# Optimization experiments

Measured on AMD Instinct MI355X. Metric: run time of the kernel, lower is better.

## Reference

```python
import jax, jax.numpy as jnp
import numpy as np

B, T, E = 4, 2048, 1024
N, P = 16, 64  # num_heads, projection_dim = E // N
SCALE = P ** 0.5


def setup_inputs() -> dict:
    key = jax.random.key(0)
    k1, k2, k3 = jax.random.split(key, 3)
    x = jax.random.normal(k1, (B, T, E), dtype=jnp.float32)
    w_qkv = jax.random.normal(k2, (E, N, 3 * P), dtype=jnp.float32) * 0.02
    b_qkv = jnp.zeros((N, 3 * P), dtype=jnp.float32)
    w_o = jax.random.normal(k3, (P, N, E), dtype=jnp.float32) * 0.02
    b_o = jnp.zeros((E,), dtype=jnp.float32)
    return {"x": x, "w_qkv": w_qkv, "b_qkv": b_qkv, "w_o": w_o, "b_o": b_o}


def reference(x, w_qkv, b_qkv, w_o, b_o):
    # QKV projection: bte,enp->btnp (+ bias over n,p)
    qkv = jnp.einsum('bte,enp->btnp', x, w_qkv) + b_qkv  # [B,T,N,3P]
    qkv = jnp.transpose(qkv, (0, 2, 1, 3))               # [B,N,T,3P]
    q, k, v = jnp.split(qkv, 3, axis=-1)                 # each [B,N,T,P]
    scores = jnp.einsum('bnip,bnjp->bnij', q, k) / SCALE # [B,N,T,T]
    attn = jax.nn.softmax(scores, axis=-1)
    weighted = jnp.einsum('bnij,bnjp->bnip', attn, v)    # [B,N,T,P]
    # Output projection: bntp,pne->bte (+ bias over e)
    out = jnp.einsum('bntp,pne->bte', weighted, w_o) + b_o
    return out
```

## Files before the change

kernel.cpp:

```cpp
#include <hip/hip_runtime.h>

typedef __attribute__((ext_vector_type(8))) short bf16x8;
typedef __attribute__((ext_vector_type(4))) short s16x4;
typedef __attribute__((ext_vector_type(4))) float f32x4;
typedef __attribute__((ext_vector_type(2))) unsigned u32x2;

#define MFMA16(a,b,c) __builtin_amdgcn_mfma_f32_16x16x32_bf16((a),(b),(c),0,0,0)

static constexpr int Bsz = 4, T = 2048, E = 1024, NH = 16, HP = 64;
static constexpr int J3 = NH * 3 * HP;

__device__ __forceinline__ short f2bf(float f) {
  union { float f; unsigned u; } v; v.f = f;
  unsigned r = (v.u + 0x7fffu + ((v.u >> 16) & 1u)) >> 16;
  return (short)r;
}

__device__ __forceinline__ unsigned cvtpk(float a, float b) {
  unsigned r;
  asm("v_cvt_pk_bf16_f32 %0, %1, %2" : "=v"(r) : "v"(a), "v"(b));
  return r;
}

typedef __attribute__((address_space(3))) unsigned int lds_u32;
typedef __attribute__((address_space(1))) const unsigned int glb_u32;
__device__ __forceinline__ void gl16(const short* g, const short* l) {
  __builtin_amdgcn_global_load_lds((glb_u32*)g, (lds_u32*)l, 16, 0, 0);
}

__global__ void cvt_x(const float4* __restrict__ x, s16x4* __restrict__ xb) {
  int i = blockIdx.x * 256 + threadIdx.x;
  float4 v = x[i];
  s16x4 r;
  r[0] = f2bf(v.x); r[1] = f2bf(v.y); r[2] = f2bf(v.z); r[3] = f2bf(v.w);
  xb[i] = r;
}

__global__ void cvt_wqkv(const float* __restrict__ w, short* __restrict__ wt) {
  __shared__ float tile[32][33];
  int jb = blockIdx.x * 32, eb = blockIdx.y * 32;
  int tx = threadIdx.x & 31, ty = threadIdx.x >> 5;
  for (int r = 0; r < 32; r += 8)
    tile[ty + r][tx] = w[(size_t)(eb + ty + r) * J3 + jb + tx];
  __syncthreads();
  for (int r = 0; r < 32; r += 8)
    wt[(size_t)(jb + ty + r) * E + eb + tx] = f2bf(tile[tx][ty + r]);
}

__global__ void cvt_wo(const float* __restrict__ w, short* __restrict__ wt) {
  int o = blockIdx.x * 256 + threadIdx.x;
  int e = o >> 10, k = o & 1023;
  int n = k >> 6, p = k & 63;
  wt[o] = f2bf(w[(size_t)(p * 16 + n) * E + e]);
}

__global__ __launch_bounds__(256) void gemm_qkv(
    const short* __restrict__ A,
    const short* __restrict__ Bt,
    const float* __restrict__ bias,
    short* __restrict__ Qb, short* __restrict__ Kb, short* __restrict__ Vt) {
  __shared__ short As[128 * 64];
  __shared__ short Bs[128 * 64];
  const int m0 = blockIdx.x * 128, n0 = blockIdx.y * 128;
  const int tid = threadIdx.x;
  const int lane = tid & 63, w = tid >> 6;
  const int wm = (w >> 1) * 64, wn = (w & 1) * 64;
  const int l15 = lane & 15, lh = lane >> 4;
  const int l7 = l15 & 7;

  const int rA = lane >> 3;
  const int cS = 8 * ((lane & 7) ^ rA);
  const short* Ap = A + (size_t)(m0 + w * 32 + rA) * 1024 + cS;
  const short* Bp = Bt + (size_t)(n0 + w * 32 + rA) * 1024 + cS;
  const short* AsBase = As + w * 2048;
  const short* BsBase = Bs + w * 2048;

  f32x4 acc[4][4] = {};

  for (int k0 = 0; k0 < 1024; k0 += 64) {
    __syncthreads();
#pragma unroll
    for (int j = 0; j < 4; j++) {
      gl16(Ap + j * 8192 + k0, AsBase + j * 512);
      gl16(Bp + j * 8192 + k0, BsBase + j * 512);
    }
    __syncthreads();
    bf16x8 af[2][4], bfr[2][4];
#pragma unroll
    for (int kk = 0; kk < 2; kk++) {
#pragma unroll
      for (int m = 0; m < 4; m++)
        af[kk][m] = *(const bf16x8*)(As + (wm + m * 16 + l15) * 64 + 8 * ((kk * 4 + lh) ^ l7));
#pragma unroll
      for (int n = 0; n < 4; n++)
        bfr[kk][n] = *(const bf16x8*)(Bs + (wn + n * 16 + l15) * 64 + 8 * ((kk * 4 + lh) ^ l7));
    }
#pragma unroll
    for (int m = 0; m < 4; m++)
#pragma unroll
      for (int n = 0; n < 4; n++) {
        acc[m][n] = MFMA16(af[0][m], bfr[0][n], acc[m][n]);
        acc[m][n] = MFMA16(af[1][m], bfr[1][n], acc[m][n]);
      }
  }

#pragma unroll
  for (int nn = 0; nn < 4; nn++) {
    int j = n0 + wn + nn * 16 + l15;
    int nh = j / 192, c = j - nh * 192;
    int ty = c >> 6, p = c & 63;
    float bv = bias[j];
#pragma unroll
    for (int mm = 0; mm < 4; mm++) {
#pragma unroll
      for (int r = 0; r < 4; r++) {
        int i = m0 + wm + mm * 16 + lh * 4 + r;
        int bb = i >> 11, tt = i & 2047;
        float val = acc[mm][nn][r] + bv;
        size_t qk = (((size_t)(bb * 16 + nh) * 2048 + tt) << 6) + p;
        if (ty == 0)      Qb[qk] = f2bf(val * 0.180336880f);
        else if (ty == 1) Kb[qk] = f2bf(val);
        else Vt[(((size_t)(bb * 16 + nh) << 6) + p) * 2048 + tt] = f2bf(val);
      }
    }
  }
}

__global__ __launch_bounds__(512, 4) void attn(
    const short* __restrict__ Qb, const short* __restrict__ Kb,
    const short* __restrict__ Vt, short* __restrict__ Wt) {
  __shared__ short Kl[2][64 * 64];
  __shared__ short Vl[2][64 * 64];
  __shared__ short Pl[8][2][16 * 64];
  const int bid = blockIdx.x;
  const int bn = bid & 63, qc = bid >> 6;
  const int tid = threadIdx.x, lane = tid & 63, w = tid >> 6;
  const int l15 = lane & 15, lh = lane >> 4;
  const int l7 = l15 & 7;
  const int q0 = qc * 256 + w * 32;

  const short* Qp = Qb + ((size_t)bn * 2048 + q0) * 64;
  const int rA = lane >> 3;
  const int cS = 8 * ((lane & 7) ^ rA);
  const short* Kg = Kb + (size_t)bn * 2048 * 64 + (w * 8 + rA) * 64 + cS;
  const short* Vg = Vt + (size_t)bn * 64 * 2048 + (size_t)(w * 8 + rA) * 2048 + cS;

  bf16x8 qf[2][2];
#pragma unroll
  for (int qg = 0; qg < 2; qg++)
#pragma unroll
    for (int c = 0; c < 2; c++)
      qf[qg][c] = *(const bf16x8*)(Qp + (qg * 16 + l15) * 64 + c * 32 + 8 * lh);

  float m[2] = {-1e30f, -1e30f}, l[2] = {0.f, 0.f};
  f32x4 o[4][2] = {};
  const f32x4 zero = {0.f, 0.f, 0.f, 0.f};

  gl16(Kg, &Kl[0][w * 512]);
  gl16(Vg, &Vl[0][w * 512]);
  __syncthreads();

  for (int t = 0; t < 32; t++) {
    const int cur = t & 1;
    if (t < 31) {
      gl16(Kg + (t + 1) * 4096, &Kl[cur ^ 1][w * 512]);
      gl16(Vg + (t + 1) * 64,   &Vl[cur ^ 1][w * 512]);
    }
    const short* Kc = &Kl[cur][0];
    const short* Vc = &Vl[cur][0];

    f32x4 s[4][2];
#pragma unroll
    for (int sub = 0; sub < 4; sub++) {
      const short* kr = Kc + (sub * 16 + l15) * 64;
      bf16x8 k0 = *(const bf16x8*)(kr + 8 * (lh ^ l7));
      bf16x8 k1 = *(const bf16x8*)(kr + 8 * ((4 + lh) ^ l7));
#pragma unroll
      for (int qg = 0; qg < 2; qg++) {
        f32x4 tt = MFMA16(k0, qf[qg][0], zero);
        s[sub][qg] = MFMA16(k1, qf[qg][1], tt);
      }
    }

#pragma unroll
    for (int qg = 0; qg < 2; qg++) {
      float pmax = fmaxf(fmaxf(s[0][qg][0], s[0][qg][1]), fmaxf(s[0][qg][2], s[0][qg][3]));
#pragma unroll
      for (int sub = 1; sub < 4; sub++)
        pmax = fmaxf(pmax, fmaxf(fmaxf(s[sub][qg][0], s[sub][qg][1]),
                                 fmaxf(s[sub][qg][2], s[sub][qg][3])));
      pmax = fmaxf(pmax, __shfl_xor(pmax, 16, 64));
      pmax = fmaxf(pmax, __shfl_xor(pmax, 32, 64));
      if (!__all(pmax - m[qg] <= 8.f)) {
        float mn = fmaxf(m[qg], pmax);
        float corr = __builtin_amdgcn_exp2f(m[qg] - mn);
        m[qg] = mn;
        l[qg] *= corr;
#pragma unroll
        for (int psub = 0; psub < 4; psub++)
#pragma unroll
          for (int r = 0; r < 4; r++) o[psub][qg][r] *= corr;
      }
      char* Pw = (char*)&Pl[w][qg][0] + l15 * 128;
      float ps = 0.f;
#pragma unroll
      for (int sub = 0; sub < 4; sub++) {
        float pv0 = __builtin_amdgcn_exp2f(s[sub][qg][0] - m[qg]);
        float pv1 = __builtin_amdgcn_exp2f(s[sub][qg][1] - m[qg]);
        float pv2 = __builtin_amdgcn_exp2f(s[sub][qg][2] - m[qg]);
        float pv3 = __builtin_amdgcn_exp2f(s[sub][qg][3] - m[qg]);
        ps += (pv0 + pv1) + (pv2 + pv3);
        u32x2 pk = {cvtpk(pv0, pv1), cvtpk(pv2, pv3)};
        *(u32x2*)(Pw + ((sub * 32 + lh * 8) ^ (l7 << 4))) = pk;
      }
      ps += __shfl_xor(ps, 16, 64);
      ps += __shfl_xor(ps, 32, 64);
      l[qg] += ps;
    }

    bf16x8 pa[2][2];
#pragma unroll
    for (int qg = 0; qg < 2; qg++) {
      const short* pr = &Pl[w][qg][0] + l15 * 64;
      pa[qg][0] = *(const bf16x8*)(pr + 8 * (lh ^ l7));
      pa[qg][1] = *(const bf16x8*)(pr + 8 * ((4 + lh) ^ l7));
    }
#pragma unroll
    for (int psub = 0; psub < 4; psub++) {
      const short* vr = Vc + (psub * 16 + l15) * 64;
      bf16x8 v0 = *(const bf16x8*)(vr + 8 * (lh ^ l7));
      bf16x8 v1 = *(const bf16x8*)(vr + 8 * ((4 + lh) ^ l7));
#pragma unroll
      for (int qg = 0; qg < 2; qg++) {
        o[psub][qg] = MFMA16(v0, pa[qg][0], o[psub][qg]);
        o[psub][qg] = MFMA16(v1, pa[qg][1], o[psub][qg]);
      }
    }
    __syncthreads();
  }

  const int bb = bn >> 4, n = bn & 15;
#pragma unroll
  for (int qg = 0; qg < 2; qg++) {
    const float invl = 1.0f / l[qg];
    short* wrow = Wt + (size_t)(bb * 2048 + q0 + qg * 16 + l15) * 1024 + n * 64;
#pragma unroll
    for (int psub = 0; psub < 4; psub++) {
      s16x4 pk;
#pragma unroll
      for (int r = 0; r < 4; r++) pk[r] = f2bf(o[psub][qg][r] * invl);
      *(s16x4*)(wrow + psub * 16 + lh * 4) = pk;
    }
  }
}

__global__ __launch_bounds__(256) void gemm_o(
    const short* __restrict__ A,
    const short* __restrict__ Bt,
    const float* __restrict__ bo,
    float* __restrict__ out) {
  __shared__ short As[128 * 64];
  __shared__ short Bs[128 * 64];
  const int m0 = blockIdx.x * 128, n0 = blockIdx.y * 128;
  const int tid = threadIdx.x;
  const int lane = tid & 63, w = tid >> 6;
  const int wm = (w >> 1) * 64, wn = (w & 1) * 64;
  const int l15 = lane & 15, lh = lane >> 4;
  const int l7 = l15 & 7;

  const int rA = lane >> 3;
  const int cS = 8 * ((lane & 7) ^ rA);
  const short* Ap = A + (size_t)(m0 + w * 32 + rA) * 1024 + cS;
  const short* Bp = Bt + (size_t)(n0 + w * 32 + rA) * 1024 + cS;
  const short* AsBase = As + w * 2048;
  const short* BsBase = Bs + w * 2048;

  f32x4 acc[4][4] = {};

  for (int k0 = 0; k0 < 1024; k0 += 64) {
    __syncthreads();
#pragma unroll
    for (int j = 0; j < 4; j++) {
      gl16(Ap + j * 8192 + k0, AsBase + j * 512);
      gl16(Bp + j * 8192 + k0, BsBase + j * 512);
    }
    __syncthreads();
    bf16x8 af[2][4], bfr[2][4];
#pragma unroll
    for (int kk = 0; kk < 2; kk++) {
#pragma unroll
      for (int m = 0; m < 4; m++)
        af[kk][m] = *(const bf16x8*)(As + (wm + m * 16 + l15) * 64 + 8 * ((kk * 4 + lh) ^ l7));
#pragma unroll
      for (int n = 0; n < 4; n++)
        bfr[kk][n] = *(const bf16x8*)(Bs + (wn + n * 16 + l15) * 64 + 8 * ((kk * 4 + lh) ^ l7));
    }
#pragma unroll
    for (int m = 0; m < 4; m++)
#pragma unroll
      for (int n = 0; n < 4; n++) {
        acc[m][n] = MFMA16(af[0][m], bfr[0][n], acc[m][n]);
        acc[m][n] = MFMA16(af[1][m], bfr[1][n], acc[m][n]);
      }
  }

#pragma unroll
  for (int nn = 0; nn < 4; nn++) {
    int e = n0 + wn + nn * 16 + l15;
    float bv = bo[e];
#pragma unroll
    for (int mm = 0; mm < 4; mm++) {
#pragma unroll
      for (int r = 0; r < 4; r++) {
        int i = m0 + wm + mm * 16 + lh * 4 + r;
        out[(size_t)i * 1024 + e] = acc[mm][nn][r] + bv;
      }
    }
  }
}

extern "C" void kernel_launch(void* const* d_in, const int* in_sizes, int n_in,
                              void* d_out, int out_size, void* d_ws, size_t ws_size,
                              hipStream_t stream) {
  (void)in_sizes; (void)n_in; (void)out_size; (void)ws_size;
  const float* x     = (const float*)d_in[0];
  const float* w_qkv = (const float*)d_in[1];
  const float* b_qkv = (const float*)d_in[2];
  const float* w_o   = (const float*)d_in[3];
  const float* b_o   = (const float*)d_in[4];
  float* out = (float*)d_out;
  char* ws = (char*)d_ws;

  short* xb     = (short*)(ws);
  short* wqkvbT = (short*)(ws + 16777216);
  short* wobT   = (short*)(ws + 23068672);
  short* Qb     = (short*)(ws + 25165824);
  short* Kb     = (short*)(ws + 41943040);
  short* Vt     = (short*)(ws + 58720256);
  short* Wt     = (short*)(ws + 75497472);

  hipLaunchKernelGGL(cvt_x,    dim3(8192),    dim3(256), 0, stream, (const float4*)x, (s16x4*)xb);
  hipLaunchKernelGGL(cvt_wqkv, dim3(96, 32),  dim3(256), 0, stream, w_qkv, wqkvbT);
  hipLaunchKernelGGL(cvt_wo,   dim3(4096),    dim3(256), 0, stream, w_o, wobT);
  hipLaunchKernelGGL(gemm_qkv, dim3(64, 24),  dim3(256), 0, stream, xb, wqkvbT, b_qkv, Qb, Kb, Vt);
  hipLaunchKernelGGL(attn,     dim3(512),     dim3(512), 0, stream, Qb, Kb, Vt, Wt);
  hipLaunchKernelGGL(gemm_o,   dim3(64, 8),   dim3(256), 0, stream, Wt, wobT, b_o, out);
}
```

Baseline: 205.4 us.

## Double-buffer LDS tiles in projection GEMMs and raise MFMA wave priority

```diff
diff --git a/kernel.cpp b/kernel.cpp
--- a/kernel.cpp
+++ b/kernel.cpp
@@ -59,8 +59,8 @@
     const short* __restrict__ Bt,
     const float* __restrict__ bias,
     short* __restrict__ Qb, short* __restrict__ Kb, short* __restrict__ Vt) {
-  __shared__ short As[128 * 64];
-  __shared__ short Bs[128 * 64];
+  __shared__ short As[2][128 * 64];
+  __shared__ short Bs[2][128 * 64];
   const int m0 = blockIdx.x * 128, n0 = blockIdx.y * 128;
   const int tid = threadIdx.x;
   const int lane = tid & 63, w = tid >> 6;
@@ -72,29 +72,39 @@
   const int cS = 8 * ((lane & 7) ^ rA);
   const short* Ap = A + (size_t)(m0 + w * 32 + rA) * 1024 + cS;
   const short* Bp = Bt + (size_t)(n0 + w * 32 + rA) * 1024 + cS;
-  const short* AsBase = As + w * 2048;
-  const short* BsBase = Bs + w * 2048;
 
   f32x4 acc[4][4] = {};
 
-  for (int k0 = 0; k0 < 1024; k0 += 64) {
-    __syncthreads();
-#pragma unroll
-    for (int j = 0; j < 4; j++) {
-      gl16(Ap + j * 8192 + k0, AsBase + j * 512);
-      gl16(Bp + j * 8192 + k0, BsBase + j * 512);
-    }
-    __syncthreads();
+#pragma unroll
+  for (int j = 0; j < 4; j++) {
+    gl16(Ap + j * 8192, &As[0][w * 2048 + j * 512]);
+    gl16(Bp + j * 8192, &Bs[0][w * 2048 + j * 512]);
+  }
+  __syncthreads();
+
+  for (int t = 0; t < 16; t++) {
+    const int cur = t & 1;
+    if (t < 15) {
+      const int k0 = (t + 1) * 64;
+#pragma unroll
+      for (int j = 0; j < 4; j++) {
+        gl16(Ap + j * 8192 + k0, &As[cur ^ 1][w * 2048 + j * 512]);
+        gl16(Bp + j * 8192 + k0, &Bs[cur ^ 1][w * 2048 + j * 512]);
+      }
+    }
+    const short* Ac = &As[cur][0];
+    const short* Bc = &Bs[cur][0];
     bf16x8 af[2][4], bfr[2][4];
 #pragma unroll
     for (int kk = 0; kk < 2; kk++) {
 #pragma unroll
       for (int m = 0; m < 4; m++)
-        af[kk][m] = *(const bf16x8*)(As + (wm + m * 16 + l15) * 64 + 8 * ((kk * 4 + lh) ^ l7));
+        af[kk][m] = *(const bf16x8*)(Ac + (wm + m * 16 + l15) * 64 + 8 * ((kk * 4 + lh) ^ l7));
 #pragma unroll
       for (int n = 0; n < 4; n++)
-        bfr[kk][n] = *(const bf16x8*)(Bs + (wn + n * 16 + l15) * 64 + 8 * ((kk * 4 + lh) ^ l7));
-    }
+        bfr[kk][n] = *(const bf16x8*)(Bc + (wn + n * 16 + l15) * 64 + 8 * ((kk * 4 + lh) ^ l7));
+    }
+    __builtin_amdgcn_s_setprio(1);
 #pragma unroll
     for (int m = 0; m < 4; m++)
 #pragma unroll
@@ -102,6 +112,8 @@
         acc[m][n] = MFMA16(af[0][m], bfr[0][n], acc[m][n]);
         acc[m][n] = MFMA16(af[1][m], bfr[1][n], acc[m][n]);
       }
+    __builtin_amdgcn_s_setprio(0);
+    __syncthreads();
   }
 
 #pragma unroll
@@ -170,6 +182,7 @@
     const short* Vc = &Vl[cur][0];
 
     f32x4 s[4][2];
+    __builtin_amdgcn_s_setprio(1);
 #pragma unroll
     for (int sub = 0; sub < 4; sub++) {
       const short* kr = Kc + (sub * 16 + l15) * 64;
@@ -181,6 +194,7 @@
         s[sub][qg] = MFMA16(k1, qf[qg][1], tt);
       }
     }
+    __builtin_amdgcn_s_setprio(0);
 
 #pragma unroll
     for (int qg = 0; qg < 2; qg++) {
@@ -225,6 +239,7 @@
       pa[qg][0] = *(const bf16x8*)(pr + 8 * (lh ^ l7));
       pa[qg][1] = *(const bf16x8*)(pr + 8 * ((4 + lh) ^ l7));
     }
+    __builtin_amdgcn_s_setprio(1);
 #pragma unroll
     for (int psub = 0; psub < 4; psub++) {
       const short* vr = Vc + (psub * 16 + l15) * 64;
@@ -236,6 +251,7 @@
         o[psub][qg] = MFMA16(v1, pa[qg][1], o[psub][qg]);
       }
     }
+    __builtin_amdgcn_s_setprio(0);
     __syncthreads();
   }
 
@@ -259,8 +275,8 @@
     const short* __restrict__ Bt,
     const float* __restrict__ bo,
     float* __restrict__ out) {
-  __shared__ short As[128 * 64];
-  __shared__ short Bs[128 * 64];
+  __shared__ short As[2][128 * 64];
+  __shared__ short Bs[2][128 * 64];
   const int m0 = blockIdx.x * 128, n0 = blockIdx.y * 128;
   const int tid = threadIdx.x;
   const int lane = tid & 63, w = tid >> 6;
@@ -272,29 +288,39 @@
   const int cS = 8 * ((lane & 7) ^ rA);
   const short* Ap = A + (size_t)(m0 + w * 32 + rA) * 1024 + cS;
   const short* Bp = Bt + (size_t)(n0 + w * 32 + rA) * 1024 + cS;
-  const short* AsBase = As + w * 2048;
-  const short* BsBase = Bs + w * 2048;
 
   f32x4 acc[4][4] = {};
 
-  for (int k0 = 0; k0 < 1024; k0 += 64) {
-    __syncthreads();
-#pragma unroll
-    for (int j = 0; j < 4; j++) {
-      gl16(Ap + j * 8192 + k0, AsBase + j * 512);
-      gl16(Bp + j * 8192 + k0, BsBase + j * 512);
-    }
-    __syncthreads();
+#pragma unroll
+  for (int j = 0; j < 4; j++) {
+    gl16(Ap + j * 8192, &As[0][w * 2048 + j * 512]);
+    gl16(Bp + j * 8192, &Bs[0][w * 2048 + j * 512]);
+  }
+  __syncthreads();
+
+  for (int t = 0; t < 16; t++) {
+    const int cur = t & 1;
+    if (t < 15) {
+      const int k0 = (t + 1) * 64;
+#pragma unroll
+      for (int j = 0; j < 4; j++) {
+        gl16(Ap + j * 8192 + k0, &As[cur ^ 1][w * 2048 + j * 512]);
+        gl16(Bp + j * 8192 + k0, &Bs[cur ^ 1][w * 2048 + j * 512]);
+      }
+    }
+    const short* Ac = &As[cur][0];
+    const short* Bc = &Bs[cur][0];
     bf16x8 af[2][4], bfr[2][4];
 #pragma unroll
     for (int kk = 0; kk < 2; kk++) {
 #pragma unroll
       for (int m = 0; m < 4; m++)
-        af[kk][m] = *(const bf16x8*)(As + (wm + m * 16 + l15) * 64 + 8 * ((kk * 4 + lh) ^ l7));
+        af[kk][m] = *(const bf16x8*)(Ac + (wm + m * 16 + l15) * 64 + 8 * ((kk * 4 + lh) ^ l7));
 #pragma unroll
       for (int n = 0; n < 4; n++)
-        bfr[kk][n] = *(const bf16x8*)(Bs + (wn + n * 16 + l15) * 64 + 8 * ((kk * 4 + lh) ^ l7));
-    }
+        bfr[kk][n] = *(const bf16x8*)(Bc + (wn + n * 16 + l15) * 64 + 8 * ((kk * 4 + lh) ^ l7));
+    }
+    __builtin_amdgcn_s_setprio(1);
 #pragma unroll
     for (int m = 0; m < 4; m++)
 #pragma unroll
@@ -302,6 +328,8 @@
         acc[m][n] = MFMA16(af[0][m], bfr[0][n], acc[m][n]);
         acc[m][n] = MFMA16(af[1][m], bfr[1][n], acc[m][n]);
       }
+    __builtin_amdgcn_s_setprio(0);
+    __syncthreads();
   }
 
 #pragma unroll
```

After: 212.0 us. +3.2%, slower.

## Double-buffer GEMM LDS tiles with register prefetch and padded rows

Applied to the files above, without the earlier changes.

```diff
diff --git a/kernel.cpp b/kernel.cpp
--- a/kernel.cpp
+++ b/kernel.cpp
@@ -59,49 +59,50 @@
     const short* __restrict__ Bt,
     const float* __restrict__ bias,
     short* __restrict__ Qb, short* __restrict__ Kb, short* __restrict__ Vt) {
-  __shared__ short As[128 * 64];
-  __shared__ short Bs[128 * 64];
+  __shared__ short As[2][128 * 40];
+  __shared__ short Bs[2][128 * 40];
   const int m0 = blockIdx.x * 128, n0 = blockIdx.y * 128;
   const int tid = threadIdx.x;
   const int lane = tid & 63, w = tid >> 6;
   const int wm = (w >> 1) * 64, wn = (w & 1) * 64;
   const int l15 = lane & 15, lh = lane >> 4;
-  const int l7 = l15 & 7;
-
-  const int rA = lane >> 3;
-  const int cS = 8 * ((lane & 7) ^ rA);
-  const short* Ap = A + (size_t)(m0 + w * 32 + rA) * 1024 + cS;
-  const short* Bp = Bt + (size_t)(n0 + w * 32 + rA) * 1024 + cS;
-  const short* AsBase = As + w * 2048;
-  const short* BsBase = Bs + w * 2048;
-
+  const int srow = tid >> 1, soff = (tid & 1) * 16;
+
+  const short* Ap = A + (size_t)(m0 + srow) * 1024 + soff;
+  const short* Bp = Bt + (size_t)(n0 + srow) * 1024 + soff;
   f32x4 acc[4][4] = {};
 
-  for (int k0 = 0; k0 < 1024; k0 += 64) {
+  bf16x8 ra0 = *(const bf16x8*)(Ap);
+  bf16x8 ra1 = *(const bf16x8*)(Ap + 8);
+  bf16x8 rb0 = *(const bf16x8*)(Bp);
+  bf16x8 rb1 = *(const bf16x8*)(Bp + 8);
+
+  for (int t = 0; t < 32; t++) {
+    const int cur = t & 1;
+    *(bf16x8*)(&As[cur][srow * 40 + soff]) = ra0;
+    *(bf16x8*)(&As[cur][srow * 40 + soff + 8]) = ra1;
+    *(bf16x8*)(&Bs[cur][srow * 40 + soff]) = rb0;
+    *(bf16x8*)(&Bs[cur][srow * 40 + soff + 8]) = rb1;
+    if (t < 31) {
+      const int k0 = (t + 1) * 32;
+      ra0 = *(const bf16x8*)(Ap + k0);
+      ra1 = *(const bf16x8*)(Ap + k0 + 8);
+      rb0 = *(const bf16x8*)(Bp + k0);
+      rb1 = *(const bf16x8*)(Bp + k0 + 8);
+    }
     __syncthreads();
-#pragma unroll
-    for (int j = 0; j < 4; j++) {
-      gl16(Ap + j * 8192 + k0, AsBase + j * 512);
-      gl16(Bp + j * 8192 + k0, BsBase + j * 512);
-    }
-    __syncthreads();
-    bf16x8 af[2][4], bfr[2][4];
-#pragma unroll
-    for (int kk = 0; kk < 2; kk++) {
-#pragma unroll
-      for (int m = 0; m < 4; m++)
-        af[kk][m] = *(const bf16x8*)(As + (wm + m * 16 + l15) * 64 + 8 * ((kk * 4 + lh) ^ l7));
+    bf16x8 af[4], bfr[4];
+#pragma unroll
+    for (int m = 0; m < 4; m++)
+      af[m] = *(const bf16x8*)(&As[cur][(wm + m * 16 + l15) * 40 + 8 * lh]);
+#pragma unroll
+    for (int n = 0; n < 4; n++)
+      bfr[n] = *(const bf16x8*)(&Bs[cur][(wn + n * 16 + l15) * 40 + 8 * lh]);
+#pragma unroll
+    for (int m = 0; m < 4; m++)
 #pragma unroll
       for (int n = 0; n < 4; n++)
-        bfr[kk][n] = *(const bf16x8*)(Bs + (wn + n * 16 + l15) * 64 + 8 * ((kk * 4 + lh) ^ l7));
-    }
-#pragma unroll
-    for (int m = 0; m < 4; m++)
-#pragma unroll
-      for (int n = 0; n < 4; n++) {
-        acc[m][n] = MFMA16(af[0][m], bfr[0][n], acc[m][n]);
-        acc[m][n] = MFMA16(af[1][m], bfr[1][n], acc[m][n]);
-      }
+        acc[m][n] = MFMA16(af[m], bfr[n], acc[m][n]);
   }
 
 #pragma unroll
@@ -259,49 +260,50 @@
     const short* __restrict__ Bt,
     const float* __restrict__ bo,
     float* __restrict__ out) {
-  __shared__ short As[128 * 64];
-  __shared__ short Bs[128 * 64];
+  __shared__ short As[2][128 * 40];
+  __shared__ short Bs[2][128 * 40];
   const int m0 = blockIdx.x * 128, n0 = blockIdx.y * 128;
   const int tid = threadIdx.x;
   const int lane = tid & 63, w = tid >> 6;
   const int wm = (w >> 1) * 64, wn = (w & 1) * 64;
   const int l15 = lane & 15, lh = lane >> 4;
-  const int l7 = l15 & 7;
-
-  const int rA = lane >> 3;
-  const int cS = 8 * ((lane & 7) ^ rA);
-  const short* Ap = A + (size_t)(m0 + w * 32 + rA) * 1024 + cS;
-  const short* Bp = Bt + (size_t)(n0 + w * 32 + rA) * 1024 + cS;
-  const short* AsBase = As + w * 2048;
-  const short* BsBase = Bs + w * 2048;
-
+  const int srow = tid >> 1, soff = (tid & 1) * 16;
+
+  const short* Ap = A + (size_t)(m0 + srow) * 1024 + soff;
+  const short* Bp = Bt + (size_t)(n0 + srow) * 1024 + soff;
   f32x4 acc[4][4] = {};
 
-  for (int k0 = 0; k0 < 1024; k0 += 64) {
+  bf16x8 ra0 = *(const bf16x8*)(Ap);
+  bf16x8 ra1 = *(const bf16x8*)(Ap + 8);
+  bf16x8 rb0 = *(const bf16x8*)(Bp);
+  bf16x8 rb1 = *(const bf16x8*)(Bp + 8);
+
+  for (int t = 0; t < 32; t++) {
+    const int cur = t & 1;
+    *(bf16x8*)(&As[cur][srow * 40 + soff]) = ra0;
+    *(bf16x8*)(&As[cur][srow * 40 + soff + 8]) = ra1;
+    *(bf16x8*)(&Bs[cur][srow * 40 + soff]) = rb0;
+    *(bf16x8*)(&Bs[cur][srow * 40 + soff + 8]) = rb1;
+    if (t < 31) {
+      const int k0 = (t + 1) * 32;
+      ra0 = *(const bf16x8*)(Ap + k0);
+      ra1 = *(const bf16x8*)(Ap + k0 + 8);
+      rb0 = *(const bf16x8*)(Bp + k0);
+      rb1 = *(const bf16x8*)(Bp + k0 + 8);
+    }
     __syncthreads();
-#pragma unroll
-    for (int j = 0; j < 4; j++) {
-      gl16(Ap + j * 8192 + k0, AsBase + j * 512);
-      gl16(Bp + j * 8192 + k0, BsBase + j * 512);
-    }
-    __syncthreads();
-    bf16x8 af[2][4], bfr[2][4];
-#pragma unroll
-    for (int kk = 0; kk < 2; kk++) {
-#pragma unroll
-      for (int m = 0; m < 4; m++)
-        af[kk][m] = *(const bf16x8*)(As + (wm + m * 16 + l15) * 64 + 8 * ((kk * 4 + lh) ^ l7));
+    bf16x8 af[4], bfr[4];
+#pragma unroll
+    for (int m = 0; m < 4; m++)
+      af[m] = *(const bf16x8*)(&As[cur][(wm + m * 16 + l15) * 40 + 8 * lh]);
+#pragma unroll
+    for (int n = 0; n < 4; n++)
+      bfr[n] = *(const bf16x8*)(&Bs[cur][(wn + n * 16 + l15) * 40 + 8 * lh]);
+#pragma unroll
+    for (int m = 0; m < 4; m++)
 #pragma unroll
       for (int n = 0; n < 4; n++)
-        bfr[kk][n] = *(const bf16x8*)(Bs + (wn + n * 16 + l15) * 64 + 8 * ((kk * 4 + lh) ^ l7));
-    }
-#pragma unroll
-    for (int m = 0; m < 4; m++)
-#pragma unroll
-      for (int n = 0; n < 4; n++) {
-        acc[m][n] = MFMA16(af[0][m], bfr[0][n], acc[m][n]);
-        acc[m][n] = MFMA16(af[1][m], bfr[1][n], acc[m][n]);
-      }
+        acc[m][n] = MFMA16(af[m], bfr[n], acc[m][n]);
   }
 
 #pragma unroll
```

Result: slower. 219.9 us (+7.1%).

## Use 32x32 MFMA in attention and keep P in registers via permlane swap

Applied to the files above, without the earlier changes.

```diff
diff --git a/kernel.cpp b/kernel.cpp
--- a/kernel.cpp
+++ b/kernel.cpp
@@ -3,9 +3,10 @@
 typedef __attribute__((ext_vector_type(8))) short bf16x8;
 typedef __attribute__((ext_vector_type(4))) short s16x4;
 typedef __attribute__((ext_vector_type(4))) float f32x4;
-typedef __attribute__((ext_vector_type(2))) unsigned u32x2;
+typedef __attribute__((ext_vector_type(16))) float f32x16;
 
 #define MFMA16(a,b,c) __builtin_amdgcn_mfma_f32_16x16x32_bf16((a),(b),(c),0,0,0)
+#define MFMA32(a,b,c) __builtin_amdgcn_mfma_f32_32x32x16_bf16((a),(b),(c),0,0,0)
 
 static constexpr int Bsz = 4, T = 2048, E = 1024, NH = 16, HP = 64;
 static constexpr int J3 = NH * 3 * HP;
@@ -131,12 +132,10 @@
     const short* __restrict__ Vt, short* __restrict__ Wt) {
   __shared__ short Kl[2][64 * 64];
   __shared__ short Vl[2][64 * 64];
-  __shared__ short Pl[8][2][16 * 64];
   const int bid = blockIdx.x;
   const int bn = bid & 63, qc = bid >> 6;
   const int tid = threadIdx.x, lane = tid & 63, w = tid >> 6;
-  const int l15 = lane & 15, lh = lane >> 4;
-  const int l7 = l15 & 7;
+  const int l31 = lane & 31, hi = lane >> 5, r7 = l31 & 7;
   const int q0 = qc * 256 + w * 32;
 
   const short* Qp = Qb + ((size_t)bn * 2048 + q0) * 64;
@@ -145,16 +144,14 @@
   const short* Kg = Kb + (size_t)bn * 2048 * 64 + (w * 8 + rA) * 64 + cS;
   const short* Vg = Vt + (size_t)bn * 64 * 2048 + (size_t)(w * 8 + rA) * 2048 + cS;
 
-  bf16x8 qf[2][2];
-#pragma unroll
-  for (int qg = 0; qg < 2; qg++)
-#pragma unroll
-    for (int c = 0; c < 2; c++)
-      qf[qg][c] = *(const bf16x8*)(Qp + (qg * 16 + l15) * 64 + c * 32 + 8 * lh);
-
-  float m[2] = {-1e30f, -1e30f}, l[2] = {0.f, 0.f};
-  f32x4 o[4][2] = {};
-  const f32x4 zero = {0.f, 0.f, 0.f, 0.f};
+  bf16x8 qf[4];
+#pragma unroll
+  for (int kseg = 0; kseg < 4; kseg++)
+    qf[kseg] = *(const bf16x8*)(Qp + l31 * 64 + kseg * 16 + hi * 8);
+
+  float m = -1e30f, l = 0.f;
+  f32x16 o0 = {}, o1 = {};
+  const f32x16 zero16 = {};
 
   gl16(Kg, &Kl[0][w * 512]);
   gl16(Vg, &Vl[0][w * 512]);
@@ -169,88 +166,94 @@
     const short* Kc = &Kl[cur][0];
     const short* Vc = &Vl[cur][0];
 
-    f32x4 s[4][2];
-#pragma unroll
-    for (int sub = 0; sub < 4; sub++) {
-      const short* kr = Kc + (sub * 16 + l15) * 64;
-      bf16x8 k0 = *(const bf16x8*)(kr + 8 * (lh ^ l7));
-      bf16x8 k1 = *(const bf16x8*)(kr + 8 * ((4 + lh) ^ l7));
-#pragma unroll
-      for (int qg = 0; qg < 2; qg++) {
-        f32x4 tt = MFMA16(k0, qf[qg][0], zero);
-        s[sub][qg] = MFMA16(k1, qf[qg][1], tt);
-      }
-    }
-
-#pragma unroll
-    for (int qg = 0; qg < 2; qg++) {
-      float pmax = fmaxf(fmaxf(s[0][qg][0], s[0][qg][1]), fmaxf(s[0][qg][2], s[0][qg][3]));
-#pragma unroll
-      for (int sub = 1; sub < 4; sub++)
-        pmax = fmaxf(pmax, fmaxf(fmaxf(s[sub][qg][0], s[sub][qg][1]),
-                                 fmaxf(s[sub][qg][2], s[sub][qg][3])));
-      pmax = fmaxf(pmax, __shfl_xor(pmax, 16, 64));
-      pmax = fmaxf(pmax, __shfl_xor(pmax, 32, 64));
-      if (!__all(pmax - m[qg] <= 8.f)) {
-        float mn = fmaxf(m[qg], pmax);
-        float corr = __builtin_amdgcn_exp2f(m[qg] - mn);
-        m[qg] = mn;
-        l[qg] *= corr;
-#pragma unroll
-        for (int psub = 0; psub < 4; psub++)
-#pragma unroll
-          for (int r = 0; r < 4; r++) o[psub][qg][r] *= corr;
-      }
-      char* Pw = (char*)&Pl[w][qg][0] + l15 * 128;
-      float ps = 0.f;
-#pragma unroll
-      for (int sub = 0; sub < 4; sub++) {
-        float pv0 = __builtin_amdgcn_exp2f(s[sub][qg][0] - m[qg]);
-        float pv1 = __builtin_amdgcn_exp2f(s[sub][qg][1] - m[qg]);
-        float pv2 = __builtin_amdgcn_exp2f(s[sub][qg][2] - m[qg]);
-        float pv3 = __builtin_amdgcn_exp2f(s[sub][qg][3] - m[qg]);
-        ps += (pv0 + pv1) + (pv2 + pv3);
-        u32x2 pk = {cvtpk(pv0, pv1), cvtpk(pv2, pv3)};
-        *(u32x2*)(Pw + ((sub * 32 + lh * 8) ^ (l7 << 4))) = pk;
-      }
-      ps += __shfl_xor(ps, 16, 64);
-      ps += __shfl_xor(ps, 32, 64);
-      l[qg] += ps;
-    }
-
-    bf16x8 pa[2][2];
-#pragma unroll
-    for (int qg = 0; qg < 2; qg++) {
-      const short* pr = &Pl[w][qg][0] + l15 * 64;
-      pa[qg][0] = *(const bf16x8*)(pr + 8 * (lh ^ l7));
-      pa[qg][1] = *(const bf16x8*)(pr + 8 * ((4 + lh) ^ l7));
-    }
-#pragma unroll
-    for (int psub = 0; psub < 4; psub++) {
-      const short* vr = Vc + (psub * 16 + l15) * 64;
-      bf16x8 v0 = *(const bf16x8*)(vr + 8 * (lh ^ l7));
-      bf16x8 v1 = *(const bf16x8*)(vr + 8 * ((4 + lh) ^ l7));
-#pragma unroll
-      for (int qg = 0; qg < 2; qg++) {
-        o[psub][qg] = MFMA16(v0, pa[qg][0], o[psub][qg]);
-        o[psub][qg] = MFMA16(v1, pa[qg][1], o[psub][qg]);
-      }
-    }
-    __syncthreads();
-  }
-
+    f32x16 s0 = zero16, s1 = zero16;
+#pragma unroll
+    for (int kseg = 0; kseg < 4; kseg++) {
+      bf16x8 k0 = *(const bf16x8*)(Kc + l31 * 64 + 8 * ((kseg * 2 + hi) ^ r7));
+      s0 = MFMA32(k0, qf[kseg], s0);
+    }
+#pragma unroll
+    for (int kseg = 0; kseg < 4; kseg++) {
+      bf16x8 k1 = *(const bf16x8*)(Kc + (32 + l31) * 64 + 8 * ((kseg * 2 + hi) ^ ((32 + l31) & 7)));
+      s1 = MFMA32(k1, qf[kseg], s1);
+    }
+
+    float pmax = fmaxf(s0[0], s0[1]);
+#pragma unroll
+    for (int r = 2; r < 16; r++) pmax = fmaxf(pmax, s0[r]);
+#pragma unroll
+    for (int r = 0; r < 16; r++) pmax = fmaxf(pmax, s1[r]);
+    pmax = fmaxf(pmax, __shfl_xor(pmax, 32, 64));
+    if (!__all(pmax - m <= 8.f)) {
+      float mn = fmaxf(m, pmax);
+      float corr = __builtin_amdgcn_exp2f(m - mn);
+      m = mn;
+      l *= corr;
+#pragma unroll
+      for (int r = 0; r < 16; r++) { o0[r] *= corr; o1[r] *= corr; }
+    }
+    float p0[16], p1[16], ps = 0.f;
+#pragma unroll
+    for (int r = 0; r < 16; r++) {
+      p0[r] = __builtin_amdgcn_exp2f(s0[r] - m);
+      p1[r] = __builtin_amdgcn_exp2f(s1[r] - m);
+      ps += p0[r] + p1[r];
+    }
+    ps += __shfl_xor(ps, 32, 64);
+    l += ps;
+
+    unsigned wk0[8], wk1[8];
+#pragma unroll
+    for (int rr = 0; rr < 4; rr++) {
+#pragma unroll
+      for (int rp = 0; rp < 2; rp++) {
+        wk0[rr * 2 + rp] = cvtpk(p0[rr * 4 + 2 * rp], p0[rr * 4 + 2 * rp + 1]);
+        wk1[rr * 2 + rp] = cvtpk(p1[rr * 4 + 2 * rp], p1[rr * 4 + 2 * rp + 1]);
+      }
+    }
+    union U8 { unsigned u[4]; bf16x8 v; };
+    bf16x8 pb[4];
+#pragma unroll
+    for (int kseg = 0; kseg < 4; kseg++) {
+      const int rrA = 2 * (kseg & 1);
+      U8 u;
+#pragma unroll
+      for (int rp = 0; rp < 2; rp++) {
+        unsigned a = (kseg < 2) ? wk0[rrA * 2 + rp] : wk1[rrA * 2 + rp];
+        unsigned b = (kseg < 2) ? wk0[(rrA + 1) * 2 + rp] : wk1[(rrA + 1) * 2 + rp];
+        asm("v_permlane32_swap_b32 %0, %1" : "+v"(a), "+v"(b));
+        u.u[rp] = a;
+        u.u[2 + rp] = b;
+      }
+      pb[kseg] = u.v;
+    }
+
+#pragma unroll
+    for (int kseg = 0; kseg < 4; kseg++) {
+      bf16x8 v0 = *(const bf16x8*)(Vc + l31 * 64 + 8 * ((kseg * 2 + hi) ^ r7));
+      o0 = MFMA32(v0, pb[kseg], o0);
+    }
+#pragma unroll
+    for (int kseg = 0; kseg < 4; kseg++) {
+      bf16x8 v1 = *(const bf16x8*)(Vc + (32 + l31) * 64 + 8 * ((kseg * 2 + hi) ^ ((32 + l31) & 7)));
+      o1 = MFMA32(v1, pb[kseg], o1);
+    }
+    __syncthreads();
+  }
+
+  const float invl = 1.0f / l;
   const int bb = bn >> 4, n = bn & 15;
-#pragma unroll
-  for (int qg = 0; qg < 2; qg++) {
-    const float invl = 1.0f / l[qg];
-    short* wrow = Wt + (size_t)(bb * 2048 + q0 + qg * 16 + l15) * 1024 + n * 64;
-#pragma unroll
-    for (int psub = 0; psub < 4; psub++) {
-      s16x4 pk;
-#pragma unroll
-      for (int r = 0; r < 4; r++) pk[r] = f2bf(o[psub][qg][r] * invl);
-      *(s16x4*)(wrow + psub * 16 + lh * 4) = pk;
-    }
+  short* wrow = Wt + (size_t)(bb * 2048 + q0 + l31) * 1024 + n * 64;
+#pragma unroll
+  for (int rr = 0; rr < 4; rr++) {
+    s16x4 pk0, pk1;
+#pragma unroll
+    for (int j = 0; j < 4; j++) {
+      pk0[j] = f2bf(o0[rr * 4 + j] * invl);
+      pk1[j] = f2bf(o1[rr * 4 + j] * invl);
+    }
+    *(s16x4*)(wrow + 8 * rr + 4 * hi) = pk0;
+    *(s16x4*)(wrow + 32 + 8 * rr + 4 * hi) = pk1;
   }
 }
 
```

Result: faster. 198.1 us (-3.6%).
